# Performance work log

Measured on AMD Instinct MI355X. Metric: run time of the kernel, lower is better.

## Reference

```python
import jax, jax.numpy as jnp
import numpy as np

PAD = 1
STRIDE = 1


def setup_inputs() -> dict:
    key = jax.random.key(0)
    k1, k2 = jax.random.split(key)
    B, C, H, W = 16, 64, 112, 112
    KS, O = 3, 128
    x = jax.random.normal(k1, (B, C, H, W), dtype=jnp.float32)
    # weight layout matches torch module: (in_channel, k, k, out_channel)
    weight = jax.random.normal(k2, (C, KS, KS, O), dtype=jnp.float32)
    return {"x": x, "weight": weight}


def reference(x, weight):
    # Original: pad -> im2col (B,Ho,Wo,C*k*k) -> matmul with weight.reshape(-1,O)
    # -> permute to (B,O,Ho,Wo). This is exactly a standard conv2d; we express
    # it as the fused implicit-GEMM convolution (same math, no huge intermediate).
    # Note: the module's _bias parameter is never used in forward, so no bias here.
    w_oihw = jnp.transpose(weight, (3, 0, 1, 2))  # (O, C, kh, kw)
    out = jax.lax.conv_general_dilated(
        x,
        w_oihw,
        window_strides=(STRIDE, STRIDE),
        padding=[(PAD, PAD), (PAD, PAD)],
        dimension_numbers=("NCHW", "OIHW", "NCHW"),
    )
    return out  # (B, O, Ho, Wo)
```

## Files before the change

### kernel.cpp

```cpp
#include <hip/hip_runtime.h>
#include <hip/hip_bf16.h>
#include <stdint.h>

typedef __attribute__((ext_vector_type(8))) short short8;
typedef __attribute__((ext_vector_type(4))) float f32x4;

#define B_   16
#define C_   64
#define H_   112
#define W_   112
#define O_   128
#define HP   114
#define HWP  (HP*HP)
#define HW   (H_*W_)
#define XPAD_BYTES ((size_t)B_*HWP*C_*2)
#define NROWS 384

__device__ __forceinline__ unsigned short f2bf(float f) {
    union { float f; uint32_t u; } v; v.f = f;
    uint32_t u = v.u;
    u += 0x7fffu + ((u >> 16) & 1u);
    return (unsigned short)(u >> 16);
}

__global__ void pad_transpose(const float* __restrict__ x,
                              unsigned short* __restrict__ xpad)
{
    __shared__ float tile[64][113];
    const int bh = blockIdx.x;
    const int b = bh / H_, h = bh % H_;
    const int t = threadIdx.x;

    const float* xr = x + ((size_t)b * C_ * HW) + (size_t)h * W_;
    #pragma unroll
    for (int i = 0; i < 28; ++i) {
        int flat = i * 256 + t;
        int c = flat / W_, w = flat % W_;
        tile[c][w] = xr[(size_t)c * HW + w];
    }

    if (t < 64) {
        size_t base = ((size_t)(b * HP + h + 1) * HP) * 64;
        xpad[base + t] = 0;
        xpad[base + (size_t)113 * 64 + t] = 0;
    }
    if (h == 0 || h == 111) {
        const int row = (h == 0) ? 0 : 113;
        size_t base = ((size_t)(b * HP + row) * HP) * 64;
        ushort4 z4; z4.x = z4.y = z4.z = z4.w = 0;
        for (int k = t; k < (HP * 64) / 4; k += 256)
            *(ushort4*)(xpad + base + (size_t)k * 4) = z4;
    }
    __syncthreads();

    unsigned short* dst = xpad + ((size_t)(b * HP + h + 1) * HP + 1) * C_;
    #pragma unroll
    for (int j = 0; j < 7; ++j) {
        int flat = j * 256 + t;
        int w = flat >> 4, c = (flat & 15) * 4;
        ushort4 v;
        v.x = f2bf(tile[c + 0][w]);
        v.y = f2bf(tile[c + 1][w]);
        v.z = f2bf(tile[c + 2][w]);
        v.w = f2bf(tile[c + 3][w]);
        *(ushort4*)(dst + (size_t)w * C_ + c) = v;
    }
}

__global__ void wtrans(const float* __restrict__ wt, unsigned short* __restrict__ wbuf)
{
    int f = blockIdx.x * 256 + threadIdx.x;
    int j    = f & 7;
    int lane = (f >> 3) & 63;
    int nf   = (f >> 9) & 3;
    int wc   = (f >> 11) & 1;
    int ks   = (f >> 12) & 1;
    int s    = f >> 13;
    int o = wc * 64 + nf * 16 + (lane & 15);
    int c = (ks * 4 + (lane >> 4)) * 8 + j;
    int kh = s / 3, kw = s % 3;
    wbuf[f] = f2bf(wt[(((size_t)c * 3 + kh) * 3 + kw) * O_ + o]);
}

__global__ __launch_bounds__(256, 3) void conv_gemm(
    const char* __restrict__ xpad,
    const char* __restrict__ wbuf,
    float* __restrict__ out)
{
    __shared__ char ldsA[NROWS * 128];

    const int t = threadIdx.x;
    const int lane = t & 63, wid = t >> 6;
    const int wr = wid >> 1, wc = wid & 1;
    const int bid0 = blockIdx.x;
    const int bid = (bid0 & 7) * 196 + (bid0 >> 3);
    const int b = bid / 98;
    const int ml0 = (bid % 98) * 128;
    const int oh0 = ml0 / W_;
    const int pbase = ml0 + 2 * oh0;

    const char* plane = xpad + (size_t)b * ((size_t)HWP * 128);
    #pragma unroll
    for (int i = 0; i < 12; ++i) {
        const int gbase = i * 256 + wid * 64;
        const int g = gbase + lane;
        const int r = g >> 3, ck = g & 7;
        __builtin_amdgcn_global_load_lds(
            (const __attribute__((address_space(1))) void*)
                (plane + (size_t)(pbase + r) * 128 + ((ck ^ (r & 7)) << 4)),
            (__attribute__((address_space(3))) void*)(ldsA + gbase * 16),
            16, 0, 0);
    }
    __syncthreads();

    int rowb[4];
    #pragma unroll
    for (int mf = 0; mf < 4; ++mf) {
        int ml = ml0 + wr * 64 + mf * 16 + (lane & 15);
        int oh = ml / W_;
        rowb[mf] = ml + 2 * oh - pbase;
    }
    const int kq = lane >> 4;

    f32x4 acc[4][4] = {};

    #pragma unroll
    for (int s = 0; s < 9; ++s) {
        const int kh = s / 3, kw = s % 3;
        const int soff = kh * HP + kw;
        const char* wb = (const char*)wbuf + s * 16384 + wc * 4096 + lane * 16;

        #pragma unroll
        for (int ks = 0; ks < 2; ++ks) {
            short8 bv[4];
            #pragma unroll
            for (int nf = 0; nf < 4; ++nf)
                bv[nf] = *(const short8*)(wb + ks * 8192 + nf * 1024);

            short8 av[4];
            #pragma unroll
            for (int mf = 0; mf < 4; ++mf) {
                const int lrow = rowb[mf] + soff;
                const int ck = (ks * 4 + kq) ^ (lrow & 7);
                av[mf] = *(const short8*)(ldsA + lrow * 128 + (ck << 4));
            }
            __builtin_amdgcn_s_setprio(1);
            #pragma unroll
            for (int mf = 0; mf < 4; ++mf)
                #pragma unroll
                for (int nf = 0; nf < 4; ++nf)
                    acc[mf][nf] = __builtin_amdgcn_mfma_f32_16x16x32_bf16(
                        av[mf], bv[nf], acc[mf][nf], 0, 0, 0);
            __builtin_amdgcn_s_setprio(0);
        }
    }

    const int oc = wc * 64 + (lane & 15);
    const int mrow = ml0 + wr * 64 + ((lane >> 4) << 2);
    #pragma unroll
    for (int mf = 0; mf < 4; ++mf) {
        #pragma unroll
        for (int nf = 0; nf < 4; ++nf) {
            float* dst = out + ((size_t)(b * O_ + oc + nf * 16) * HW) + mrow + mf * 16;
            *(f32x4*)dst = acc[mf][nf];
        }
    }
}

extern "C" void kernel_launch(void* const* d_in, const int* in_sizes, int n_in,
                              void* d_out, int out_size, void* d_ws, size_t ws_size,
                              hipStream_t stream) {
    const float* x  = (const float*)d_in[0];
    const float* wt = (const float*)d_in[1];
    float* out = (float*)d_out;
    char* xpad = (char*)d_ws;
    char* wbuf = (char*)d_ws + XPAD_BYTES;

    hipLaunchKernelGGL(pad_transpose, dim3(B_ * H_), dim3(256), 0, stream,
                       x, (unsigned short*)xpad);
    hipLaunchKernelGGL(wtrans, dim3(288), dim3(256), 0, stream,
                       wt, (unsigned short*)wbuf);
    hipLaunchKernelGGL(conv_gemm, dim3(1568), dim3(256), 0, stream,
                       xpad, wbuf, out);
}
```

Measured before the change: 64.73 us.

## Fuse padding and bf16 conversion into conv GEMM loader, drop pad kernel

Removes the separate pad_transpose kernel and its bf16 NHWC workspace. The conv_gemm kernel now reads fp32 NCHW input directly, applies zero-padding via bounds checks, converts to bf16 with packed cvt instructions, and writes the swizzled tile into LDS. This eliminates one launch and a full round trip of the padded tensor through global memory. The cost is strided, uncoalesced per-channel loads (8 loads 12544 floats apart per thread), redundant reads of halo rows across blocks, and occupancy lowered from 3 to 2 blocks.

After: 88.58 us. 1.37x slower.

```diff
diff --git a/kernel.cpp b/kernel.cpp
--- a/kernel.cpp
+++ b/kernel.cpp
@@ -13,58 +13,13 @@
 #define HP   114
 #define HWP  (HP*HP)
 #define HW   (H_*W_)
-#define XPAD_BYTES ((size_t)B_*HWP*C_*2)
-#define NROWS 384
+#define NROWS 362
 
 __device__ __forceinline__ unsigned short f2bf(float f) {
     union { float f; uint32_t u; } v; v.f = f;
     uint32_t u = v.u;
     u += 0x7fffu + ((u >> 16) & 1u);
     return (unsigned short)(u >> 16);
-}
-
-__global__ void pad_transpose(const float* __restrict__ x,
-                              unsigned short* __restrict__ xpad)
-{
-    __shared__ float tile[64][113];
-    const int bh = blockIdx.x;
-    const int b = bh / H_, h = bh % H_;
-    const int t = threadIdx.x;
-
-    const float* xr = x + ((size_t)b * C_ * HW) + (size_t)h * W_;
-    #pragma unroll
-    for (int i = 0; i < 28; ++i) {
-        int flat = i * 256 + t;
-        int c = flat / W_, w = flat % W_;
-        tile[c][w] = xr[(size_t)c * HW + w];
-    }
-
-    if (t < 64) {
-        size_t base = ((size_t)(b * HP + h + 1) * HP) * 64;
-        xpad[base + t] = 0;
-        xpad[base + (size_t)113 * 64 + t] = 0;
-    }
-    if (h == 0 || h == 111) {
-        const int row = (h == 0) ? 0 : 113;
-        size_t base = ((size_t)(b * HP + row) * HP) * 64;
-        ushort4 z4; z4.x = z4.y = z4.z = z4.w = 0;
-        for (int k = t; k < (HP * 64) / 4; k += 256)
-            *(ushort4*)(xpad + base + (size_t)k * 4) = z4;
-    }
-    __syncthreads();
-
-    unsigned short* dst = xpad + ((size_t)(b * HP + h + 1) * HP + 1) * C_;
-    #pragma unroll
-    for (int j = 0; j < 7; ++j) {
-        int flat = j * 256 + t;
-        int w = flat >> 4, c = (flat & 15) * 4;
-        ushort4 v;
-        v.x = f2bf(tile[c + 0][w]);
-        v.y = f2bf(tile[c + 1][w]);
-        v.z = f2bf(tile[c + 2][w]);
-        v.w = f2bf(tile[c + 3][w]);
-        *(ushort4*)(dst + (size_t)w * C_ + c) = v;
-    }
 }
 
 __global__ void wtrans(const float* __restrict__ wt, unsigned short* __restrict__ wbuf)
@@ -82,8 +37,8 @@
     wbuf[f] = f2bf(wt[(((size_t)c * 3 + kh) * 3 + kw) * O_ + o]);
 }
 
-__global__ __launch_bounds__(256, 3) void conv_gemm(
-    const char* __restrict__ xpad,
+__global__ __launch_bounds__(256, 2) void conv_gemm(
+    const float* __restrict__ x,
     const char* __restrict__ wbuf,
     float* __restrict__ out)
 {
@@ -99,17 +54,28 @@
     const int oh0 = ml0 / W_;
     const int pbase = ml0 + 2 * oh0;
 
-    const char* plane = xpad + (size_t)b * ((size_t)HWP * 128);
-    #pragma unroll
+    const float* xb = x + (size_t)b * C_ * HW;
+    #pragma unroll 4
     for (int i = 0; i < 12; ++i) {
-        const int gbase = i * 256 + wid * 64;
-        const int g = gbase + lane;
-        const int r = g >> 3, ck = g & 7;
-        __builtin_amdgcn_global_load_lds(
-            (const __attribute__((address_space(1))) void*)
-                (plane + (size_t)(pbase + r) * 128 + ((ck ^ (r & 7)) << 4)),
-            (__attribute__((address_space(3))) void*)(ldsA + gbase * 16),
-            16, 0, 0);
+        const int idx = i * 256 + t;
+        if (i < 11 || idx < 2896) {
+            const int r = idx >> 3, pos = idx & 7;
+            const int p = pbase + r;
+            const int ph = p / HP, pw = p - ph * HP;
+            union { uint32_t u[4]; short8 s; } v;
+            v.u[0] = v.u[1] = v.u[2] = v.u[3] = 0;
+            if (ph >= 1 && ph <= 112 && pw >= 1 && pw <= 112) {
+                const float* src = xb + (size_t)((pos ^ (r & 7)) * 8) * HW
+                                 + (ph - 1) * W_ + (pw - 1);
+                float f0 = src[0],      f1 = src[HW],     f2 = src[2*HW], f3 = src[3*HW];
+                float f4 = src[4*HW],   f5 = src[5*HW],   f6 = src[6*HW], f7 = src[7*HW];
+                asm("v_cvt_pk_bf16_f32 %0, %1, %2" : "=v"(v.u[0]) : "v"(f0), "v"(f1));
+                asm("v_cvt_pk_bf16_f32 %0, %1, %2" : "=v"(v.u[1]) : "v"(f2), "v"(f3));
+                asm("v_cvt_pk_bf16_f32 %0, %1, %2" : "=v"(v.u[2]) : "v"(f4), "v"(f5));
+                asm("v_cvt_pk_bf16_f32 %0, %1, %2" : "=v"(v.u[3]) : "v"(f6), "v"(f7));
+            }
+            *(short8*)(ldsA + (size_t)idx * 16) = v.s;
+        }
     }
     __syncthreads();
 
@@ -126,9 +92,8 @@
 
     #pragma unroll
     for (int s = 0; s < 9; ++s) {
-        const int kh = s / 3, kw = s % 3;
-        const int soff = kh * HP + kw;
-        const char* wb = (const char*)wbuf + s * 16384 + wc * 4096 + lane * 16;
+        const int soff = (s / 3) * HP + (s % 3);
+        const char* wb = wbuf + s * 16384 + wc * 4096 + lane * 16;
 
         #pragma unroll
         for (int ks = 0; ks < 2; ++ks) {
@@ -173,13 +138,10 @@
     const float* x  = (const float*)d_in[0];
     const float* wt = (const float*)d_in[1];
     float* out = (float*)d_out;
-    char* xpad = (char*)d_ws;
-    char* wbuf = (char*)d_ws + XPAD_BYTES;
+    char* wbuf = (char*)d_ws;
 
-    hipLaunchKernelGGL(pad_transpose, dim3(B_ * H_), dim3(256), 0, stream,
-                       x, (unsigned short*)xpad);
     hipLaunchKernelGGL(wtrans, dim3(288), dim3(256), 0, stream,
                        wt, (unsigned short*)wbuf);
     hipLaunchKernelGGL(conv_gemm, dim3(1568), dim3(256), 0, stream,
-                       xpad, wbuf, out);
+                       x, wbuf, out);
 }
```
